# Optimization experiments

Measured on AMD Instinct MI355X. Metric: run time of the kernel, lower is better.

Reference implementation:

```python
import jax, jax.numpy as jnp
import numpy as np

N_NODES = 40000
N_EDGES = 640000
NFEAT = 128
NHID = 64  # gc1: NFEAT -> 2*NHID, gc2: 2*NHID -> NHID


def setup_inputs() -> dict:
    key = jax.random.key(0)
    ks = jax.random.split(key, 8)
    x = jax.random.normal(ks[0], (N_NODES, NFEAT), dtype=jnp.float32)
    edge_src = jax.random.randint(ks[1], (N_EDGES,), 0, N_NODES, dtype=jnp.int32)
    edge_dst = jax.random.randint(ks[2], (N_EDGES,), 0, N_NODES, dtype=jnp.int32)
    # normalized adjacency weights (e.g. D^-1/2 A D^-1/2 values), positive
    edge_weight = jax.random.uniform(ks[3], (N_EDGES,), dtype=jnp.float32)
    # Glorot-style init as in Kipf GraphConvolution (uniform +- 1/sqrt(fan_out))
    W1 = jax.random.uniform(ks[4], (NFEAT, 2 * NHID), dtype=jnp.float32,
                            minval=-1.0 / np.sqrt(2 * NHID), maxval=1.0 / np.sqrt(2 * NHID))
    b1 = jnp.zeros((2 * NHID,), dtype=jnp.float32)
    W2 = jax.random.uniform(ks[5], (2 * NHID, NHID), dtype=jnp.float32,
                            minval=-1.0 / np.sqrt(NHID), maxval=1.0 / np.sqrt(NHID))
    b2 = jnp.zeros((NHID,), dtype=jnp.float32)
    return {"x": x, "edge_src": edge_src, "edge_dst": edge_dst,
            "edge_weight": edge_weight, "W1": W1, "b1": b1, "W2": W2, "b2": b2}


def _gcn_layer(h, edge_src, edge_dst, edge_weight, W, b, n_nodes):
    # support = h @ W  (dense GEMM), then out = spmm(adj, support) + b
    support = h @ W                                   # [N, Dout]
    msgs = edge_weight[:, None] * support[edge_src]   # [E, Dout] gather
    agg = jax.ops.segment_sum(msgs, edge_dst, num_segments=n_nodes)  # scatter-add
    return agg + b


def reference(x, edge_src, edge_dst, edge_weight, W1, b1, W2, b2):
    n = x.shape[0]
    # gc1 -> relu -> dropout(eval: identity) -> gc2
    h = jax.nn.relu(_gcn_layer(x, edge_src, edge_dst, edge_weight, W1, b1, n))
    out = _gcn_layer(h, edge_src, edge_dst, edge_weight, W2, b2, n)
    return out
```

## Files before the change

### kernel.cpp

```cpp
#include <hip/hip_runtime.h>

#define N_NODES 40000
#define N_EDGES 640000
#define NFEAT   128
#define H1      128
#define H2      64

#define NBUCK   625
#define BCAP    2048
#define EPB     4096
#define NBINB   157
#define HPAD    68

#define OFF_SUP1   0UL
#define OFF_SUP2   10240000UL
#define OFF_BUCK   15360000UL
#define OFF_GSRT   25600000UL
#define OFF_GNFO   30720000UL
#define OFF_GCUR   30880256UL
#define OFF_W1T    30882816UL
#define OFF_W2T    30915584UL

typedef unsigned int uint;
typedef unsigned short ushort;
typedef __attribute__((ext_vector_type(8))) short bf16x8;
typedef __attribute__((ext_vector_type(4))) float f32x4;
typedef __attribute__((ext_vector_type(2))) float f32x2;

__device__ __forceinline__ float bl(uint u) { union { uint i; float f; } c; c.i = u << 16; return c.f; }
__device__ __forceinline__ float bh(uint u) { union { uint i; float f; } c; c.i = u & 0xFFFF0000u; return c.f; }
__device__ __forceinline__ ushort f2b(float f) {
    union { float f; uint i; } c; c.f = f;
    uint u = c.i + 0x7FFFu + ((c.i >> 16) & 1u);
    return (ushort)(u >> 16);
}

__global__ void init_k(uint* __restrict__ gcur,
                       const float* __restrict__ W1, const float* __restrict__ W2,
                       ushort* __restrict__ W1T, ushort* __restrict__ W2T) {
    const int i = blockIdx.x * 256 + threadIdx.x;
    if (i < NBUCK + 1) gcur[i] = 0;
    if (i < 128 * 128) {
        const int c = i >> 7, k = i & 127;
        W1T[i] = f2b(W1[k * 128 + c]);
    }
    if (i < 64 * 128) {
        const int c = i >> 7, k = i & 127;
        W2T[i] = f2b(W2[k * 64 + c]);
    }
}

__global__ __launch_bounds__(1024) void bingemm_k(const int* __restrict__ edst,
                                                  const int* __restrict__ esrc,
                                                  const float* __restrict__ ew,
                                                  uint* __restrict__ gcur,
                                                  uint2* __restrict__ buckets,
                                                  const float* __restrict__ x,
                                                  const ushort* __restrict__ W1T,
                                                  ushort* __restrict__ sup1) {
    __shared__ uint2 stage[EPB];
    __shared__ uint cntL[NBUCK + 1];
    __shared__ uint offL[NBUCK + 1];
    __shared__ uint gbase[NBUCK + 1];
    __shared__ int wsum[16];
    const int t = threadIdx.x;
    const int lane = t & 63, wv = t >> 6;

    if (blockIdx.x >= NBINB) {
        const int gid = blockIdx.x - NBINB;
        const int m0 = gid * 256 + wv * 16;
        if (m0 >= N_NODES) return;
        const int r = lane & 15, kg = lane >> 4;

        bf16x8 a[4];
        const float* xp = x + (size_t)(m0 + r) * 128 + kg * 8;
#pragma unroll
        for (int kt = 0; kt < 4; ++kt) {
            float xf[8];
            *(float4*)(xf)     = *(const float4*)(xp + kt * 32);
            *(float4*)(xf + 4) = *(const float4*)(xp + kt * 32 + 4);
            bf16x8 v;
#pragma unroll
            for (int i = 0; i < 8; ++i) v[i] = (short)f2b(xf[i]);
            a[kt] = v;
        }
#pragma unroll
        for (int nt = 0; nt < 8; ++nt) {
            const ushort* wp = W1T + (size_t)(nt * 16 + r) * 128 + kg * 8;
            f32x4 acc = {0.f, 0.f, 0.f, 0.f};
#pragma unroll
            for (int kt = 0; kt < 4; ++kt) {
                const bf16x8 bfr = *(const bf16x8*)(wp + kt * 32);
                acc = __builtin_amdgcn_mfma_f32_16x16x32_bf16(a[kt], bfr, acc, 0, 0, 0);
            }
#pragma unroll
            for (int q = 0; q < 4; ++q)
                sup1[(size_t)(m0 + kg * 4 + q) * 128 + nt * 16 + r] = f2b(acc[q]);
        }
        return;
    }

    if (t < NBUCK + 1) cntL[t] = 0;
    __syncthreads();

    uint d_[4], rec_[4], rk_[4]; int b_[4];
#pragma unroll
    for (int k = 0; k < 4; ++k) {
        const int i = blockIdx.x * EPB + k * 1024 + t;
        uint d = 40000, rec = 0;
        if (i < N_EDGES) {
            d = (uint)edst[i];
            rec = ((uint)esrc[i] << 16) | (uint)f2b(ew[i]);
        }
        d_[k] = d; rec_[k] = rec; b_[k] = d >> 6;
        rk_[k] = atomicAdd(&cntL[b_[k]], 1u);
    }
    __syncthreads();

    {
        const int v = (t < NBUCK + 1) ? (int)cntL[t] : 0;
        int incl = v;
#pragma unroll
        for (int d = 1; d < 64; d <<= 1) {
            int o = __shfl_up(incl, d);
            if (lane >= d) incl += o;
        }
        if (lane == 63) wsum[wv] = incl;
        __syncthreads();
        if (t < 16) {
            int s = wsum[t];
#pragma unroll
            for (int d = 1; d < 16; d <<= 1) {
                int o = __shfl_up(s, d);
                if (t >= d) s += o;
            }
            wsum[t] = s;
        }
        __syncthreads();
        if (t < NBUCK + 1) {
            offL[t] = (uint)((wv ? wsum[wv - 1] : 0) + incl - v);
            gbase[t] = atomicAdd(&gcur[t], (uint)v);
        }
    }
    __syncthreads();

#pragma unroll
    for (int k = 0; k < 4; ++k) {
        uint2 s; s.x = d_[k]; s.y = rec_[k];
        stage[offL[b_[k]] + rk_[k]] = s;
    }
    __syncthreads();

#pragma unroll
    for (int k = 0; k < 4; ++k) {
        const int p = k * 1024 + t;
        const uint2 s = stage[p];
        const uint b = s.x >> 6;
        if (b < NBUCK) {
            const uint pos = gbase[b] + ((uint)p - offL[b]);
            if (pos < BCAP) buckets[(size_t)b * BCAP + pos] = s;
        }
    }
}

__global__ __launch_bounds__(1024) void spmmg_k(const ushort* __restrict__ sup,
                                                const uint* __restrict__ gcur,
                                                const uint2* __restrict__ buckets,
                                                const float* __restrict__ b1,
                                                const ushort* __restrict__ W2T,
                                                ushort* __restrict__ sup2,
                                                uint* __restrict__ gsrt,
                                                uint* __restrict__ gnfo) {
    __shared__ uint srt[BCAP];
    __shared__ uint htile[64 * HPAD];
    __shared__ uint cntL[64];
    __shared__ uint offL[64];
    const int t = threadIdx.x;
    const int bkt = blockIdx.x;
    if (t < 64) cntL[t] = 0;
    __syncthreads();

    const int cnt = min((int)gcur[bkt], BCAP);
    const uint* bp32 = (const uint*)(buckets + (size_t)bkt * BCAP);

    int n0 = -1, n1 = -1; uint rec0 = 0, rec1 = 0, rk0 = 0, rk1 = 0;
    if (t < cnt) {
        const uint dx = __builtin_nontemporal_load(&bp32[2 * t]);
        rec0 = __builtin_nontemporal_load(&bp32[2 * t + 1]);
        n0 = dx & 63; rk0 = atomicAdd(&cntL[n0], 1u);
    }
    if (t + 1024 < cnt) {
        const uint dx = __builtin_nontemporal_load(&bp32[2 * (t + 1024)]);
        rec1 = __builtin_nontemporal_load(&bp32[2 * (t + 1024) + 1]);
        n1 = dx & 63; rk1 = atomicAdd(&cntL[n1], 1u);
    }
    __syncthreads();

    if (t < 64) {
        const int v = (int)cntL[t];
        int incl = v;
#pragma unroll
        for (int d = 1; d < 64; d <<= 1) {
            int o = __shfl_up(incl, d);
            if (t >= d) incl += o;
        }
        offL[t] = (uint)(incl - v);
    }
    __syncthreads();

    if (n0 >= 0) srt[offL[n0] + rk0] = rec0;
    if (n1 >= 0) srt[offL[n1] + rk1] = rec1;
    __syncthreads();

    if (t < cnt)        gsrt[(size_t)bkt * BCAP + t]        = srt[t];
    if (t + 1024 < cnt) gsrt[(size_t)bkt * BCAP + t + 1024] = srt[t + 1024];
    if (t < 64) gnfo[bkt * 64 + t] = (offL[t] << 12) | cntL[t];

    const int lane = t & 63, wv = t >> 6;
    const uint* sup32 = (const uint*)sup;
    const float2 bb = ((const float2*)b1)[lane];
#pragma unroll
    for (int j = 0; j < 4; ++j) {
        const int n = wv * 4 + j;
        const int e0 = (int)offL[n], c = (int)cntL[n];
        float a0 = 0.f, a1 = 0.f, a2 = 0.f, a3 = 0.f;
        int e = 0;
        for (; e + 8 <= c; e += 8) {
            uint r[8], v[8];
#pragma unroll
            for (int k = 0; k < 8; ++k) r[k] = srt[e0 + e + k];
#pragma unroll
            for (int k = 0; k < 8; ++k) v[k] = sup32[((size_t)(r[k] >> 16) << 6) + lane];
#pragma unroll
            for (int k = 0; k < 8; k += 2) {
                const float w0 = bl(r[k]), w1 = bl(r[k + 1]);
                a0 = fmaf(w0, bl(v[k]), a0);     a1 = fmaf(w0, bh(v[k]), a1);
                a2 = fmaf(w1, bl(v[k + 1]), a2); a3 = fmaf(w1, bh(v[k + 1]), a3);
            }
        }
        for (; e + 4 <= c; e += 4) {
            uint r[4], v[4];
#pragma unroll
            for (int k = 0; k < 4; ++k) r[k] = srt[e0 + e + k];
#pragma unroll
            for (int k = 0; k < 4; ++k) v[k] = sup32[((size_t)(r[k] >> 16) << 6) + lane];
#pragma unroll
            for (int k = 0; k < 4; k += 2) {
                const float w0 = bl(r[k]), w1 = bl(r[k + 1]);
                a0 = fmaf(w0, bl(v[k]), a0);     a1 = fmaf(w0, bh(v[k]), a1);
                a2 = fmaf(w1, bl(v[k + 1]), a2); a3 = fmaf(w1, bh(v[k + 1]), a3);
            }
        }
        for (; e < c; ++e) {
            const uint r0 = srt[e0 + e];
            const uint v0 = sup32[((size_t)(r0 >> 16) << 6) + lane];
            a0 = fmaf(bl(r0), bl(v0), a0); a1 = fmaf(bl(r0), bh(v0), a1);
        }
        const float f0 = fmaxf((a0 + a2) + bb.x, 0.f);
        const float f1 = fmaxf((a1 + a3) + bb.y, 0.f);
        htile[n * HPAD + lane] = (uint)f2b(f0) | ((uint)f2b(f1) << 16);
    }
    __syncthreads();

    {
        const int r = lane & 15, kg = lane >> 4;
        const int rowtile = wv >> 2, ntile = wv & 3;
        const uint* hrow = htile + (rowtile * 16 + r) * HPAD + kg * 4;
        bf16x8 a[4];
#pragma unroll
        for (int kt = 0; kt < 4; ++kt) a[kt] = *(const bf16x8*)(hrow + kt * 16);

        const ushort* wp = W2T + (size_t)(ntile * 16 + r) * 128 + kg * 8;
        f32x4 acc = {0.f, 0.f, 0.f, 0.f};
#pragma unroll
        for (int kt = 0; kt < 4; ++kt) {
            const bf16x8 bfr = *(const bf16x8*)(wp + kt * 32);
            acc = __builtin_amdgcn_mfma_f32_16x16x32_bf16(a[kt], bfr, acc, 0, 0, 0);
        }
#pragma unroll
        for (int q = 0; q < 4; ++q)
            sup2[(size_t)(bkt * 64 + rowtile * 16 + kg * 4 + q) * 64 + ntile * 16 + r] = f2b(acc[q]);
    }
}

__global__ __launch_bounds__(1024) void spmm2_k(const ushort* __restrict__ sup,
                                                const uint* __restrict__ gcur,
                                                const uint* __restrict__ gsrt,
                                                const uint* __restrict__ gnfo,
                                                const float* __restrict__ b2,
                                                float* __restrict__ out) {
    __shared__ uint srt[BCAP];
    __shared__ uint cntL[64];
    __shared__ uint offL[64];
    const int t = threadIdx.x;
    const int bkt = blockIdx.x;
    const int cnt = min((int)gcur[bkt], BCAP);

    if (t < 64) {
        const uint p = gnfo[bkt * 64 + t];
        offL[t] = p >> 12;
        cntL[t] = p & 0xFFFu;
    }
    const uint* gs = gsrt + (size_t)bkt * BCAP;
    if (t < cnt)        srt[t]        = gs[t];
    if (t + 1024 < cnt) srt[t + 1024] = gs[t + 1024];
    __syncthreads();

    const int lane = t & 63, wv = t >> 6;
    const int hh = lane >> 5, l32 = lane & 31;
    const uint* sup32 = (const uint*)sup;
    const float2 bb = ((const float2*)b2)[l32];
#pragma unroll
    for (int j = 0; j < 4; ++j) {
        const int n = wv * 4 + j;
        const int e0 = (int)offL[n], c = (int)cntL[n];
        float d0 = 0.f, d1 = 0.f, d2 = 0.f, d3 = 0.f;
        int e = 0;
        for (; e + 8 <= c; e += 8) {
            const uint r0 = srt[e0 + e + hh],     r1 = srt[e0 + e + 2 + hh];
            const uint r2 = srt[e0 + e + 4 + hh], r3 = srt[e0 + e + 6 + hh];
            const uint v0 = sup32[((size_t)(r0 >> 16) << 5) + l32];
            const uint v1 = sup32[((size_t)(r1 >> 16) << 5) + l32];
            const uint v2 = sup32[((size_t)(r2 >> 16) << 5) + l32];
            const uint v3 = sup32[((size_t)(r3 >> 16) << 5) + l32];
            d0 = fmaf(bl(r0), bl(v0), d0); d1 = fmaf(bl(r0), bh(v0), d1);
            d2 = fmaf(bl(r1), bl(v1), d2); d3 = fmaf(bl(r1), bh(v1), d3);
            d0 = fmaf(bl(r2), bl(v2), d0); d1 = fmaf(bl(r2), bh(v2), d1);
            d2 = fmaf(bl(r3), bl(v3), d2); d3 = fmaf(bl(r3), bh(v3), d3);
        }
        for (; e + 2 <= c; e += 2) {
            const uint r0 = srt[e0 + e + hh];
            const uint v0 = sup32[((size_t)(r0 >> 16) << 5) + l32];
            d0 = fmaf(bl(r0), bl(v0), d0); d1 = fmaf(bl(r0), bh(v0), d1);
        }
        if (e < c && hh == 0) {
            const uint r0 = srt[e0 + e];
            const uint v0 = sup32[((size_t)(r0 >> 16) << 5) + l32];
            d0 = fmaf(bl(r0), bl(v0), d0); d1 = fmaf(bl(r0), bh(v0), d1);
        }
        float g0 = d0 + d2, g1 = d1 + d3;
        g0 += __shfl_xor(g0, 32); g1 += __shfl_xor(g1, 32);
        if (hh == 0) {
            f32x2 res = {g0 + bb.x, g1 + bb.y};
            __builtin_nontemporal_store(res, (f32x2*)out + (size_t)(bkt * 64 + n) * 32 + l32);
        }
    }
}

extern "C" void kernel_launch(void* const* d_in, const int* in_sizes, int n_in,
                              void* d_out, int out_size, void* d_ws, size_t ws_size,
                              hipStream_t stream) {
    const float* x    = (const float*)d_in[0];
    const int*   esrc = (const int*)d_in[1];
    const int*   edst = (const int*)d_in[2];
    const float* ew   = (const float*)d_in[3];
    const float* W1   = (const float*)d_in[4];
    const float* b1   = (const float*)d_in[5];
    const float* W2   = (const float*)d_in[6];
    const float* b2   = (const float*)d_in[7];
    float* out = (float*)d_out;

    char* ws = (char*)d_ws;
    ushort* sup1    = (ushort*)(ws + OFF_SUP1);
    ushort* sup2    = (ushort*)(ws + OFF_SUP2);
    uint2*  buckets = (uint2*)(ws + OFF_BUCK);
    uint*   gsrt    = (uint*)(ws + OFF_GSRT);
    uint*   gnfo    = (uint*)(ws + OFF_GNFO);
    uint*   gcur    = (uint*)(ws + OFF_GCUR);
    ushort* W1T     = (ushort*)(ws + OFF_W1T);
    ushort* W2T     = (ushort*)(ws + OFF_W2T);

    init_k<<<64, 256, 0, stream>>>(gcur, W1, W2, W1T, W2T);
    bingemm_k<<<NBINB + 157, 1024, 0, stream>>>(edst, esrc, ew, gcur, buckets, x, W1T, sup1);
    spmmg_k<<<NBUCK, 1024, 0, stream>>>(sup1, gcur, buckets, b1, W2T, sup2, gsrt, gnfo);
    spmm2_k<<<NBUCK, 1024, 0, stream>>>(sup2, gcur, gsrt, gnfo, b2, out);
}
```

Before: 81.38 us.

## Process four nodes per wave with wide vector gathers in both SpMM phases

Both aggregation phases change from one wave per node, looped over four nodes serially, to each wave handling four nodes at once with 16 lanes per node. In layer 1 each lane gathers 16 bytes (uint4) of the support row, and in layer 2 each lane gathers 8 bytes (uint2). The aim is fewer, wider memory requests and more gathers in flight per wave, so the latency-bound gather loops take fewer serial iterations. In exchange, the loop trip count now varies across the four nodes in a wave, which can cause divergence, and per-lane register use rises with the eight or four accumulators and wider loads.

```diff
diff --git a/kernel.cpp b/kernel.cpp
--- a/kernel.cpp
+++ b/kernel.cpp
@@ -25,7 +25,6 @@
 typedef unsigned short ushort;
 typedef __attribute__((ext_vector_type(8))) short bf16x8;
 typedef __attribute__((ext_vector_type(4))) float f32x4;
-typedef __attribute__((ext_vector_type(2))) float f32x2;
 
 __device__ __forceinline__ float bl(uint u) { union { uint i; float f; } c; c.i = u << 16; return c.f; }
 __device__ __forceinline__ float bh(uint u) { union { uint i; float f; } c; c.i = u & 0xFFFF0000u; return c.f; }
@@ -217,48 +216,62 @@
     if (t < 64) gnfo[bkt * 64 + t] = (offL[t] << 12) | cntL[t];
 
     const int lane = t & 63, wv = t >> 6;
-    const uint* sup32 = (const uint*)sup;
-    const float2 bb = ((const float2*)b1)[lane];
-#pragma unroll
-    for (int j = 0; j < 4; ++j) {
-        const int n = wv * 4 + j;
+    const int q = lane >> 4, ql = lane & 15;
+    const uint4* sup128 = (const uint4*)sup;
+    {
+        const int n = wv * 4 + q;
         const int e0 = (int)offL[n], c = (int)cntL[n];
-        float a0 = 0.f, a1 = 0.f, a2 = 0.f, a3 = 0.f;
+        float acc[8] = {};
         int e = 0;
         for (; e + 8 <= c; e += 8) {
-            uint r[8], v[8];
+            uint r[8]; uint4 v[8];
 #pragma unroll
             for (int k = 0; k < 8; ++k) r[k] = srt[e0 + e + k];
 #pragma unroll
-            for (int k = 0; k < 8; ++k) v[k] = sup32[((size_t)(r[k] >> 16) << 6) + lane];
-#pragma unroll
-            for (int k = 0; k < 8; k += 2) {
-                const float w0 = bl(r[k]), w1 = bl(r[k + 1]);
-                a0 = fmaf(w0, bl(v[k]), a0);     a1 = fmaf(w0, bh(v[k]), a1);
-                a2 = fmaf(w1, bl(v[k + 1]), a2); a3 = fmaf(w1, bh(v[k + 1]), a3);
+            for (int k = 0; k < 8; ++k) v[k] = sup128[((size_t)(r[k] >> 16) << 4) + ql];
+#pragma unroll
+            for (int k = 0; k < 8; ++k) {
+                const float w = bl(r[k]);
+                acc[0] = fmaf(w, bl(v[k].x), acc[0]); acc[1] = fmaf(w, bh(v[k].x), acc[1]);
+                acc[2] = fmaf(w, bl(v[k].y), acc[2]); acc[3] = fmaf(w, bh(v[k].y), acc[3]);
+                acc[4] = fmaf(w, bl(v[k].z), acc[4]); acc[5] = fmaf(w, bh(v[k].z), acc[5]);
+                acc[6] = fmaf(w, bl(v[k].w), acc[6]); acc[7] = fmaf(w, bh(v[k].w), acc[7]);
             }
         }
         for (; e + 4 <= c; e += 4) {
-            uint r[4], v[4];
+            uint r[4]; uint4 v[4];
 #pragma unroll
             for (int k = 0; k < 4; ++k) r[k] = srt[e0 + e + k];
 #pragma unroll
-            for (int k = 0; k < 4; ++k) v[k] = sup32[((size_t)(r[k] >> 16) << 6) + lane];
-#pragma unroll
-            for (int k = 0; k < 4; k += 2) {
-                const float w0 = bl(r[k]), w1 = bl(r[k + 1]);
-                a0 = fmaf(w0, bl(v[k]), a0);     a1 = fmaf(w0, bh(v[k]), a1);
-                a2 = fmaf(w1, bl(v[k + 1]), a2); a3 = fmaf(w1, bh(v[k + 1]), a3);
+            for (int k = 0; k < 4; ++k) v[k] = sup128[((size_t)(r[k] >> 16) << 4) + ql];
+#pragma unroll
+            for (int k = 0; k < 4; ++k) {
+                const float w = bl(r[k]);
+                acc[0] = fmaf(w, bl(v[k].x), acc[0]); acc[1] = fmaf(w, bh(v[k].x), acc[1]);
+                acc[2] = fmaf(w, bl(v[k].y), acc[2]); acc[3] = fmaf(w, bh(v[k].y), acc[3]);
+                acc[4] = fmaf(w, bl(v[k].z), acc[4]); acc[5] = fmaf(w, bh(v[k].z), acc[5]);
+                acc[6] = fmaf(w, bl(v[k].w), acc[6]); acc[7] = fmaf(w, bh(v[k].w), acc[7]);
             }
         }
         for (; e < c; ++e) {
             const uint r0 = srt[e0 + e];
-            const uint v0 = sup32[((size_t)(r0 >> 16) << 6) + lane];
-            a0 = fmaf(bl(r0), bl(v0), a0); a1 = fmaf(bl(r0), bh(v0), a1);
-        }
-        const float f0 = fmaxf((a0 + a2) + bb.x, 0.f);
-        const float f1 = fmaxf((a1 + a3) + bb.y, 0.f);
-        htile[n * HPAD + lane] = (uint)f2b(f0) | ((uint)f2b(f1) << 16);
+            const uint4 v0 = sup128[((size_t)(r0 >> 16) << 4) + ql];
+            const float w = bl(r0);
+            acc[0] = fmaf(w, bl(v0.x), acc[0]); acc[1] = fmaf(w, bh(v0.x), acc[1]);
+            acc[2] = fmaf(w, bl(v0.y), acc[2]); acc[3] = fmaf(w, bh(v0.y), acc[3]);
+            acc[4] = fmaf(w, bl(v0.z), acc[4]); acc[5] = fmaf(w, bh(v0.z), acc[5]);
+            acc[6] = fmaf(w, bl(v0.w), acc[6]); acc[7] = fmaf(w, bh(v0.w), acc[7]);
+        }
+        const float2 bq0 = ((const float2*)b1)[ql * 4 + 0];
+        const float2 bq1 = ((const float2*)b1)[ql * 4 + 1];
+        const float2 bq2 = ((const float2*)b1)[ql * 4 + 2];
+        const float2 bq3 = ((const float2*)b1)[ql * 4 + 3];
+        uint4 pk;
+        pk.x = (uint)f2b(fmaxf(acc[0] + bq0.x, 0.f)) | ((uint)f2b(fmaxf(acc[1] + bq0.y, 0.f)) << 16);
+        pk.y = (uint)f2b(fmaxf(acc[2] + bq1.x, 0.f)) | ((uint)f2b(fmaxf(acc[3] + bq1.y, 0.f)) << 16);
+        pk.z = (uint)f2b(fmaxf(acc[4] + bq2.x, 0.f)) | ((uint)f2b(fmaxf(acc[5] + bq2.y, 0.f)) << 16);
+        pk.w = (uint)f2b(fmaxf(acc[6] + bq3.x, 0.f)) | ((uint)f2b(fmaxf(acc[7] + bq3.y, 0.f)) << 16);
+        *(uint4*)(htile + n * HPAD + ql * 4) = pk;
     }
     __syncthreads();
 
@@ -278,8 +291,8 @@
             acc = __builtin_amdgcn_mfma_f32_16x16x32_bf16(a[kt], bfr, acc, 0, 0, 0);
         }
 #pragma unroll
-        for (int q = 0; q < 4; ++q)
-            sup2[(size_t)(bkt * 64 + rowtile * 16 + kg * 4 + q) * 64 + ntile * 16 + r] = f2b(acc[q]);
+        for (int p = 0; p < 4; ++p)
+            sup2[(size_t)(bkt * 64 + rowtile * 16 + kg * 4 + p) * 64 + ntile * 16 + r] = f2b(acc[p]);
     }
 }
 
@@ -307,44 +320,48 @@
     __syncthreads();
 
     const int lane = t & 63, wv = t >> 6;
-    const int hh = lane >> 5, l32 = lane & 31;
-    const uint* sup32 = (const uint*)sup;
-    const float2 bb = ((const float2*)b2)[l32];
-#pragma unroll
-    for (int j = 0; j < 4; ++j) {
-        const int n = wv * 4 + j;
-        const int e0 = (int)offL[n], c = (int)cntL[n];
-        float d0 = 0.f, d1 = 0.f, d2 = 0.f, d3 = 0.f;
-        int e = 0;
-        for (; e + 8 <= c; e += 8) {
-            const uint r0 = srt[e0 + e + hh],     r1 = srt[e0 + e + 2 + hh];
-            const uint r2 = srt[e0 + e + 4 + hh], r3 = srt[e0 + e + 6 + hh];
-            const uint v0 = sup32[((size_t)(r0 >> 16) << 5) + l32];
-            const uint v1 = sup32[((size_t)(r1 >> 16) << 5) + l32];
-            const uint v2 = sup32[((size_t)(r2 >> 16) << 5) + l32];
-            const uint v3 = sup32[((size_t)(r3 >> 16) << 5) + l32];
-            d0 = fmaf(bl(r0), bl(v0), d0); d1 = fmaf(bl(r0), bh(v0), d1);
-            d2 = fmaf(bl(r1), bl(v1), d2); d3 = fmaf(bl(r1), bh(v1), d3);
-            d0 = fmaf(bl(r2), bl(v2), d0); d1 = fmaf(bl(r2), bh(v2), d1);
-            d2 = fmaf(bl(r3), bl(v3), d2); d3 = fmaf(bl(r3), bh(v3), d3);
-        }
-        for (; e + 2 <= c; e += 2) {
-            const uint r0 = srt[e0 + e + hh];
-            const uint v0 = sup32[((size_t)(r0 >> 16) << 5) + l32];
-            d0 = fmaf(bl(r0), bl(v0), d0); d1 = fmaf(bl(r0), bh(v0), d1);
-        }
-        if (e < c && hh == 0) {
-            const uint r0 = srt[e0 + e];
-            const uint v0 = sup32[((size_t)(r0 >> 16) << 5) + l32];
-            d0 = fmaf(bl(r0), bl(v0), d0); d1 = fmaf(bl(r0), bh(v0), d1);
-        }
-        float g0 = d0 + d2, g1 = d1 + d3;
-        g0 += __shfl_xor(g0, 32); g1 += __shfl_xor(g1, 32);
-        if (hh == 0) {
-            f32x2 res = {g0 + bb.x, g1 + bb.y};
-            __builtin_nontemporal_store(res, (f32x2*)out + (size_t)(bkt * 64 + n) * 32 + l32);
-        }
-    }
+    const int q = lane >> 4, ql = lane & 15;
+    const uint2* sup64 = (const uint2*)sup;
+    const int n = wv * 4 + q;
+    const int e0 = (int)offL[n], c = (int)cntL[n];
+    float acc[4] = {};
+    int e = 0;
+    for (; e + 8 <= c; e += 8) {
+        uint r[8]; uint2 v[8];
+#pragma unroll
+        for (int k = 0; k < 8; ++k) r[k] = srt[e0 + e + k];
+#pragma unroll
+        for (int k = 0; k < 8; ++k) v[k] = sup64[((size_t)(r[k] >> 16) << 4) + ql];
+#pragma unroll
+        for (int k = 0; k < 8; ++k) {
+            const float w = bl(r[k]);
+            acc[0] = fmaf(w, bl(v[k].x), acc[0]); acc[1] = fmaf(w, bh(v[k].x), acc[1]);
+            acc[2] = fmaf(w, bl(v[k].y), acc[2]); acc[3] = fmaf(w, bh(v[k].y), acc[3]);
+        }
+    }
+    for (; e + 4 <= c; e += 4) {
+        uint r[4]; uint2 v[4];
+#pragma unroll
+        for (int k = 0; k < 4; ++k) r[k] = srt[e0 + e + k];
+#pragma unroll
+        for (int k = 0; k < 4; ++k) v[k] = sup64[((size_t)(r[k] >> 16) << 4) + ql];
+#pragma unroll
+        for (int k = 0; k < 4; ++k) {
+            const float w = bl(r[k]);
+            acc[0] = fmaf(w, bl(v[k].x), acc[0]); acc[1] = fmaf(w, bh(v[k].x), acc[1]);
+            acc[2] = fmaf(w, bl(v[k].y), acc[2]); acc[3] = fmaf(w, bh(v[k].y), acc[3]);
+        }
+    }
+    for (; e < c; ++e) {
+        const uint r0 = srt[e0 + e];
+        const uint2 v0 = sup64[((size_t)(r0 >> 16) << 4) + ql];
+        const float w = bl(r0);
+        acc[0] = fmaf(w, bl(v0.x), acc[0]); acc[1] = fmaf(w, bh(v0.x), acc[1]);
+        acc[2] = fmaf(w, bl(v0.y), acc[2]); acc[3] = fmaf(w, bh(v0.y), acc[3]);
+    }
+    const float4 bb = ((const float4*)b2)[ql];
+    f32x4 res = {acc[0] + bb.x, acc[1] + bb.y, acc[2] + bb.z, acc[3] + bb.w};
+    __builtin_nontemporal_store(res, (f32x4*)out + (size_t)(bkt * 64 + n) * 16 + ql);
 }
 
 extern "C" void kernel_launch(void* const* d_in, const int* in_sizes, int n_in,
```

Result: no change. 82.84 us (+1.8%).
